# Optimization experiments

Measured on AMD Instinct MI355X. Metric: run time of the kernel, lower is better.

The kernel has to match this reference:

```python
import jax, jax.numpy as jnp
import numpy as np

H = 256
LOG_STD_MIN, LOG_STD_MAX = -20.0, 2.0


def setup_inputs() -> dict:
    key = jax.random.key(0)
    ks = jax.random.split(key, 12)
    B, T, F, A = 256, 1000, 64, 16
    s_in = 1.0 / np.sqrt(H)
    inp = {
        "observations": jax.random.normal(ks[0], (B, T, F), jnp.float32),
        # LSTM params (PyTorch gate order: i, f, g, o)
        "W_ih": jax.random.uniform(ks[1], (4 * H, F), jnp.float32, -s_in, s_in),
        "W_hh": jax.random.uniform(ks[2], (4 * H, H), jnp.float32, -s_in, s_in),
        "b_ih": jax.random.uniform(ks[3], (4 * H,), jnp.float32, -s_in, s_in),
        "b_hh": jax.random.uniform(ks[4], (4 * H,), jnp.float32, -s_in, s_in),
        # layer2: Linear(256 -> 256)
        "W2": jax.random.uniform(ks[5], (H, H), jnp.float32, -s_in, s_in),
        "b2": jax.random.uniform(ks[6], (H,), jnp.float32, -s_in, s_in),
        # means head: Linear(256 -> A)
        "Wm": jax.random.uniform(ks[7], (A, H), jnp.float32, -s_in, s_in),
        "bm": jax.random.uniform(ks[8], (A,), jnp.float32, -s_in, s_in),
        # log_stds head: Linear(256 -> A)
        "Ws": jax.random.uniform(ks[9], (A, H), jnp.float32, -s_in, s_in),
        "bs": jax.random.uniform(ks[10], (A,), jnp.float32, -s_in, s_in),
    }
    return inp


def _lstm(observations, W_ih, W_hh, b_ih, b_hh):
    B, T, F = observations.shape
    # Precompute the input-to-gate projection for all timesteps: [T, B, 4H]
    xg = jnp.einsum("btf,gf->tbg", observations, W_ih) + (b_ih + b_hh)
    W_hh_T = W_hh.T  # [H, 4H]

    def step(carry, xg_t):
        h, c = carry  # [B, H] each
        gates = xg_t + h @ W_hh_T  # [B, 4H]
        i, f, g, o = jnp.split(gates, 4, axis=-1)
        i = jax.nn.sigmoid(i)
        f = jax.nn.sigmoid(f)
        g = jnp.tanh(g)
        o = jax.nn.sigmoid(o)
        c = f * c + i * g
        h = o * jnp.tanh(c)
        return (h, c), h

    h0 = jnp.zeros((B, H), observations.dtype)
    c0 = jnp.zeros((B, H), observations.dtype)
    _, hs = jax.lax.scan(step, (h0, c0), xg)  # hs: [T, B, H]
    return jnp.transpose(hs, (1, 0, 2))  # [B, T, H]


def reference(observations, W_ih, W_hh, b_ih, b_hh, W2, b2, Wm, bm, Ws, bs):
    x = _lstm(observations, W_ih, W_hh, b_ih, b_hh)  # [B, T, H]
    x = jax.nn.relu(jnp.einsum("bth,oh->bto", x, W2) + b2)  # [B, T, H]
    means = jnp.einsum("bth,ah->bta", x, Wm) + bm  # [B, T, A]
    log_stds = jnp.einsum("bth,ah->bta", x, Ws) + bs  # [B, T, A]
    stds = jnp.exp(jnp.clip(log_stds, LOG_STD_MIN, LOG_STD_MAX))
    return (means, stds)
```

## Files before the change

kernel.cpp:

```cpp
#include <hip/hip_runtime.h>


#define NB 256
#define NT 1000
#define NF 64
#define NH 256
#define NG 1024
#define NA 16
#define NTHREADS 512
#define CHUNK 8
#define NCHUNK (NT / CHUNK)
#define HHALF 68

typedef _Float16 h2 __attribute__((ext_vector_type(2)));
typedef _Float16 h4 __attribute__((ext_vector_type(4)));
typedef _Float16 h8 __attribute__((ext_vector_type(8)));
typedef float f4 __attribute__((ext_vector_type(4)));

__device__ __forceinline__ float fdot2(h2 a, h2 b, float c) {
  return __builtin_amdgcn_fdot2(a, b, c, false);
}
__device__ __forceinline__ float fexp2(float x) { return __builtin_amdgcn_exp2f(x); }
__device__ __forceinline__ float frcp(float x) { return __builtin_amdgcn_rcpf(x); }
__device__ __forceinline__ float sigmoidf_(float x) {
  return frcp(1.f + fexp2(-1.4426950408889634f * x));
}
__device__ __forceinline__ float tanhfast(float x) {
  float a = fabsf(x);
  float e = fexp2(-2.8853900817779268f * a);
  float r = (1.f - e) * frcp(1.f + e);
  return __builtin_copysignf(r, x);
}
__device__ __forceinline__ float dot8(h8 x, h8 w, float acc) {
  acc = fdot2(__builtin_shufflevector(x, x, 0, 1), __builtin_shufflevector(w, w, 0, 1), acc);
  acc = fdot2(__builtin_shufflevector(x, x, 2, 3), __builtin_shufflevector(w, w, 2, 3), acc);
  acc = fdot2(__builtin_shufflevector(x, x, 4, 5), __builtin_shufflevector(w, w, 4, 5), acc);
  acc = fdot2(__builtin_shufflevector(x, x, 6, 7), __builtin_shufflevector(w, w, 6, 7), acc);
  return acc;
}
template <int CTRL>
__device__ __forceinline__ float qperm(float x) {
  return __int_as_float(
      __builtin_amdgcn_update_dpp(0, __float_as_int(x), CTRL, 0xF, 0xF, true));
}

__global__ void prep_kernel(const float* __restrict__ Wih, const float* __restrict__ Whh,
                            const float* __restrict__ bih, const float* __restrict__ bhh,
                            const float* __restrict__ W2, const float* __restrict__ Wm,
                            const float* __restrict__ Ws,
                            h2* __restrict__ whh, h2* __restrict__ wih,
                            h2* __restrict__ w2w, h2* __restrict__ wmh,
                            float* __restrict__ bg) {
  int i = blockIdx.x * 256 + threadIdx.x;
  if (i < 1024 * 128) {
    int j = i >> 7, p = i & 127;
    whh[i] = h2{(_Float16)Whh[j * 256 + 2 * p], (_Float16)Whh[j * 256 + 2 * p + 1]};
  }
  if (i < 1024 * 32) {
    int j = i >> 5, p = i & 31;
    wih[i] = h2{(_Float16)Wih[j * 64 + 2 * p], (_Float16)Wih[j * 64 + 2 * p + 1]};
  }
  if (i < 256 * 128) {
    int j = i >> 7, p = i & 127;
    w2w[i] = h2{(_Float16)W2[j * 256 + 2 * p], (_Float16)W2[j * 256 + 2 * p + 1]};
  }
  if (i < 32 * 128) {
    int j = i >> 7, p = i & 127;
    float v0, v1;
    if (j < 16) { v0 = Wm[j * 256 + 2 * p]; v1 = Wm[j * 256 + 2 * p + 1]; }
    else        { v0 = Ws[(j - 16) * 256 + 2 * p]; v1 = Ws[(j - 16) * 256 + 2 * p + 1]; }
    wmh[i] = h2{(_Float16)v0, (_Float16)v1};
  }
  if (i < 1024) bg[i] = bih[i] + bhh[i];
}

__global__ __launch_bounds__(NTHREADS, 2) void actor_kernel(
    const float* __restrict__ obs,
    const h2* __restrict__ whh, const h2* __restrict__ wih,
    const h2* __restrict__ w2w, const h2* __restrict__ wmh,
    const float* __restrict__ bg, const float* __restrict__ b2,
    const float* __restrict__ bm, const float* __restrict__ bs,
    float* __restrict__ out) {
  __shared__ __align__(16) h8 whh_l[16 * NTHREADS];
  __shared__ __align__(16) _Float16 xg_l[CHUNK * NG];
  __shared__ __align__(16) h2 hbuf[2][2 * HHALF];
  __shared__ __align__(16) h2 hch[CHUNK * NH / 2];
  __shared__ __align__(16) h2 xbuf[CHUNK * NF / 2];
  __shared__ __align__(16) h2 x2b[CHUNK * NH / 2];

  const int tid = threadIdx.x;
  const int b = blockIdx.x;
  const int q = tid >> 1;
  const int jhalf = tid & 1;

  h8 wreg[48];
  {
    const volatile h8* vw = (const volatile h8*)whh;
#pragma unroll
    for (int g = 0; g < 4; g++)
#pragma unroll
      for (int jj = 0; jj < 12; jj++)
        wreg[g * 12 + jj] = vw[(g * 256 + q) * 32 + jhalf * 16 + 4 + jj];
  }
  {
    const h8* whh8 = (const h8*)whh;
#pragma unroll
    for (int g = 0; g < 4; g++)
#pragma unroll
      for (int s = 0; s < 4; s++)
        whh_l[(g * 4 + s) * NTHREADS + tid] = whh8[(g * 256 + q) * 32 + jhalf * 16 + s];
  }
  if (tid < 2 * HHALF) hbuf[0][tid] = h2{(_Float16)0.f, (_Float16)0.f};
  float c_state = 0.f;
  const float bg0 = bg[tid], bg1 = bg[tid + 512];
  const float b2v = b2[tid & 255];
  const int oh = tid & 31;
  const float hbv = (oh < NA) ? bm[oh] : bs[oh - NA];
  __syncthreads();

  const float* obs_b = obs + (size_t)b * NT * NF;
  float* out_means = out;
  float* out_stds = out + (size_t)NB * NT * NA;

  for (int ch = 0; ch < NCHUNK; ++ch) {
    const int t0 = ch * CHUNK;

    if (tid < 128) {
      int t = tid >> 4, fq = tid & 15;
      f4 v = *(const f4*)(obs_b + (size_t)(t0 + t) * NF + fq * 4);
      xbuf[t * 32 + fq * 2] = h2{(_Float16)v[0], (_Float16)v[1]};
      xbuf[t * 32 + fq * 2 + 1] = h2{(_Float16)v[2], (_Float16)v[3]};
    }
    __syncthreads();

#pragma unroll
    for (int rr = 0; rr < 2; ++rr) {
      const int row = tid + rr * 512;
      const float bias = rr ? bg1 : bg0;
      float acc[CHUNK];
#pragma unroll
      for (int t = 0; t < CHUNK; t++) acc[t] = bias;
      const h8* wrow = (const h8*)wih + row * 8;
#pragma unroll
      for (int jh = 0; jh < 2; jh++) {
        h8 w[4];
#pragma unroll
        for (int qq = 0; qq < 4; qq++) w[qq] = wrow[jh * 4 + qq];
#pragma unroll
        for (int t = 0; t < CHUNK; t++) {
#pragma unroll
          for (int qq = 0; qq < 4; qq++) {
            h8 xv = *(const h8*)&xbuf[t * 32 + jh * 16 + qq * 4];
            acc[t] = dot8(xv, w[qq], acc[t]);
          }
        }
      }
      const int g = row >> 8, uu = row & 255;
#pragma unroll
      for (int t = 0; t < CHUNK; t++)
        xg_l[(t * 256 + uu) * 4 + g] = (_Float16)acc[t];
    }
    __syncthreads();

    for (int t = 0; t < CHUNK; t++) {
      const _Float16* hb = (const _Float16*)&hbuf[t & 1][jhalf * HHALF];
      h4 xg4 = *(const h4*)&xg_l[(t * 256 + q) * 4];
      float p0 = 0.f, p1 = 0.f, p2 = 0.f, p3 = 0.f;
#pragma unroll
      for (int s = 0; s < 4; s++) {
        h8 hv = *(const h8*)(hb + s * 8);
        p0 = dot8(hv, whh_l[(0 * 4 + s) * NTHREADS + tid], p0);
        p1 = dot8(hv, whh_l[(1 * 4 + s) * NTHREADS + tid], p1);
        p2 = dot8(hv, whh_l[(2 * 4 + s) * NTHREADS + tid], p2);
        p3 = dot8(hv, whh_l[(3 * 4 + s) * NTHREADS + tid], p3);
      }
#pragma unroll
      for (int jj = 0; jj < 12; jj++) {
        h8 hv = *(const h8*)(hb + 32 + jj * 8);
        p0 = dot8(hv, wreg[jj], p0);
        p1 = dot8(hv, wreg[12 + jj], p1);
        p2 = dot8(hv, wreg[24 + jj], p2);
        p3 = dot8(hv, wreg[36 + jj], p3);
      }
      p0 += qperm<0xB1>(p0);
      p1 += qperm<0xB1>(p1);
      p2 += qperm<0xB1>(p2);
      p3 += qperm<0xB1>(p3);
      float gi = sigmoidf_(p0 + (float)xg4[0]);
      float gf = sigmoidf_(p1 + (float)xg4[1]);
      float gg = tanhfast(p2 + (float)xg4[2]);
      float go = sigmoidf_(p3 + (float)xg4[3]);
      c_state = gf * c_state + gi * gg;
      float hval = go * tanhfast(c_state);
      if (jhalf == 0) {
        _Float16 hh = (_Float16)hval;
        ((_Float16*)&hbuf[(t + 1) & 1][(q >> 7) * HHALF])[q & 127] = hh;
        ((_Float16*)hch)[t * NH + q] = hh;
      }
      __syncthreads();
    }

    {
      const int o = tid & 255;
      const int tb = (tid >> 8) * 4;
      float acc[4] = {b2v, b2v, b2v, b2v};
      const h8* wrow = (const h8*)w2w + o * 32;
#pragma unroll 2
      for (int c = 0; c < 8; c++) {
        h8 w[4];
#pragma unroll
        for (int qq = 0; qq < 4; qq++) w[qq] = wrow[c * 4 + qq];
#pragma unroll
        for (int tt = 0; tt < 4; tt++) {
#pragma unroll
          for (int qq = 0; qq < 4; qq++) {
            h8 xv = *(const h8*)&hch[(tb + tt) * 128 + c * 16 + qq * 4];
            acc[tt] = dot8(xv, w[qq], acc[tt]);
          }
        }
      }
#pragma unroll
      for (int tt = 0; tt < 4; tt++)
        ((_Float16*)x2b)[(tb + tt) * NH + o] = (_Float16)fmaxf(acc[tt], 0.f);
    }
    __syncthreads();

    if (tid < 256) {
      const int tt = tid >> 5;
      const h8* wrow = (const h8*)wmh + oh * 32;
      float acc = 0.f;
#pragma unroll 4
      for (int c = 0; c < 32; c++) {
        h8 xv = *(const h8*)&x2b[tt * 128 + c * 4];
        acc = dot8(xv, wrow[c], acc);
      }
      acc += hbv;
      const size_t idx = ((size_t)b * NT + (t0 + tt)) * NA + (oh & 15);
      if (oh < NA) {
        out_means[idx] = acc;
      } else {
        float ls = fminf(fmaxf(acc, -20.f), 2.f);
        out_stds[idx] = fexp2(1.4426950408889634f * ls);
      }
    }
  }
}

extern "C" void kernel_launch(void* const* d_in, const int* in_sizes, int n_in,
                              void* d_out, int out_size, void* d_ws, size_t ws_size,
                              hipStream_t stream) {
  const float* obs = (const float*)d_in[0];
  const float* Wih = (const float*)d_in[1];
  const float* Whh = (const float*)d_in[2];
  const float* bih = (const float*)d_in[3];
  const float* bhh = (const float*)d_in[4];
  const float* W2 = (const float*)d_in[5];
  const float* b2 = (const float*)d_in[6];
  const float* Wm = (const float*)d_in[7];
  const float* bm = (const float*)d_in[8];
  const float* Ws = (const float*)d_in[9];
  const float* bs = (const float*)d_in[10];

  char* ws = (char*)d_ws;
  h2* whh = (h2*)(ws + 0);
  h2* wih = (h2*)(ws + 524288);
  h2* w2w = (h2*)(ws + 655360);
  h2* wmh = (h2*)(ws + 786432);
  float* bg = (float*)(ws + 802816);

  prep_kernel<<<512, 256, 0, stream>>>(Wih, Whh, bih, bhh, W2, Wm, Ws,
                                       whh, wih, w2w, wmh, bg);
  actor_kernel<<<NB, NTHREADS, 0, stream>>>(obs, whh, wih, w2w, wmh, bg, b2, bm,
                                            bs, (float*)d_out);
}
```

Baseline: 4.554 ms.

## Process two batch sequences per block to share recurrent weights and barriers

Each workgroup now runs the LSTM recurrence for two batch rows at once, halving the grid. The recurrent weights held in registers and LDS are reused for both sequences, and each per-timestep barrier covers two sequences, which cuts total synchronisation per sequence. CHUNK drops to 4 so the LDS buffers fit. The cost is twice the dot-product work per step per block and only half the CUs occupied.

```diff
diff --git a/kernel.cpp b/kernel.cpp
--- a/kernel.cpp
+++ b/kernel.cpp
@@ -2,13 +2,14 @@
 
 
 #define NB 256
+#define GRID 128
 #define NT 1000
 #define NF 64
 #define NH 256
 #define NG 1024
 #define NA 16
 #define NTHREADS 512
-#define CHUNK 8
+#define CHUNK 4
 #define NCHUNK (NT / CHUNK)
 #define HHALF 68
 
@@ -82,11 +83,11 @@
     const float* __restrict__ bm, const float* __restrict__ bs,
     float* __restrict__ out) {
   __shared__ __align__(16) h8 whh_l[16 * NTHREADS];
-  __shared__ __align__(16) _Float16 xg_l[CHUNK * NG];
-  __shared__ __align__(16) h2 hbuf[2][2 * HHALF];
-  __shared__ __align__(16) h2 hch[CHUNK * NH / 2];
-  __shared__ __align__(16) h2 xbuf[CHUNK * NF / 2];
-  __shared__ __align__(16) h2 x2b[CHUNK * NH / 2];
+  __shared__ __align__(16) _Float16 xg_l[CHUNK * 2 * NG];
+  __shared__ __align__(16) h2 hbuf[2][2][2 * HHALF];
+  __shared__ __align__(16) h2 hch[2][CHUNK][NH / 2];
+  __shared__ __align__(16) h2 xbuf[2][CHUNK][NF / 2];
+  __shared__ __align__(16) h2 x2b[2][CHUNK][NH / 2];
 
   const int tid = threadIdx.x;
   const int b = blockIdx.x;
@@ -110,15 +111,14 @@
       for (int s = 0; s < 4; s++)
         whh_l[(g * 4 + s) * NTHREADS + tid] = whh8[(g * 256 + q) * 32 + jhalf * 16 + s];
   }
-  if (tid < 2 * HHALF) hbuf[0][tid] = h2{(_Float16)0.f, (_Float16)0.f};
-  float c_state = 0.f;
+  if (tid < 2 * 2 * HHALF) ((h2*)hbuf)[tid] = h2{(_Float16)0.f, (_Float16)0.f};
+  float c0 = 0.f, c1 = 0.f;
   const float bg0 = bg[tid], bg1 = bg[tid + 512];
   const float b2v = b2[tid & 255];
   const int oh = tid & 31;
-  const float hbv = (oh < NA) ? bm[oh] : bs[oh - NA];
+  const float headb = (oh < NA) ? bm[oh] : bs[oh - NA];
   __syncthreads();
 
-  const float* obs_b = obs + (size_t)b * NT * NF;
   float* out_means = out;
   float* out_stds = out + (size_t)NB * NT * NA;
 
@@ -126,10 +126,11 @@
     const int t0 = ch * CHUNK;
 
     if (tid < 128) {
-      int t = tid >> 4, fq = tid & 15;
-      f4 v = *(const f4*)(obs_b + (size_t)(t0 + t) * NF + fq * 4);
-      xbuf[t * 32 + fq * 2] = h2{(_Float16)v[0], (_Float16)v[1]};
-      xbuf[t * 32 + fq * 2 + 1] = h2{(_Float16)v[2], (_Float16)v[3]};
+      int rb = tid >> 6, tq = (tid >> 4) & 3, fq = tid & 15;
+      const float* ob = obs + ((size_t)(2 * b + rb) * NT + (t0 + tq)) * NF;
+      f4 v = *(const f4*)(ob + fq * 4);
+      xbuf[rb][tq][fq * 2] = h2{(_Float16)v[0], (_Float16)v[1]};
+      xbuf[rb][tq][fq * 2 + 1] = h2{(_Float16)v[2], (_Float16)v[3]};
     }
     __syncthreads();
 
@@ -137,9 +138,11 @@
     for (int rr = 0; rr < 2; ++rr) {
       const int row = tid + rr * 512;
       const float bias = rr ? bg1 : bg0;
-      float acc[CHUNK];
-#pragma unroll
-      for (int t = 0; t < CHUNK; t++) acc[t] = bias;
+      float acc[2][4];
+#pragma unroll
+      for (int rb = 0; rb < 2; rb++)
+#pragma unroll
+        for (int tq = 0; tq < 4; tq++) acc[rb][tq] = bias;
       const h8* wrow = (const h8*)wih + row * 8;
 #pragma unroll
       for (int jh = 0; jh < 2; jh++) {
@@ -147,95 +150,123 @@
 #pragma unroll
         for (int qq = 0; qq < 4; qq++) w[qq] = wrow[jh * 4 + qq];
 #pragma unroll
-        for (int t = 0; t < CHUNK; t++) {
-#pragma unroll
-          for (int qq = 0; qq < 4; qq++) {
-            h8 xv = *(const h8*)&xbuf[t * 32 + jh * 16 + qq * 4];
-            acc[t] = dot8(xv, w[qq], acc[t]);
-          }
-        }
+        for (int rb = 0; rb < 2; rb++)
+#pragma unroll
+          for (int tq = 0; tq < 4; tq++)
+#pragma unroll
+            for (int qq = 0; qq < 4; qq++) {
+              h8 xv = *(const h8*)&xbuf[rb][tq][jh * 16 + qq * 4];
+              acc[rb][tq] = dot8(xv, w[qq], acc[rb][tq]);
+            }
       }
       const int g = row >> 8, uu = row & 255;
 #pragma unroll
-      for (int t = 0; t < CHUNK; t++)
-        xg_l[(t * 256 + uu) * 4 + g] = (_Float16)acc[t];
+      for (int rb = 0; rb < 2; rb++)
+#pragma unroll
+        for (int tq = 0; tq < 4; tq++)
+          xg_l[((tq * 2 + rb) * 256 + uu) * 4 + g] = (_Float16)acc[rb][tq];
     }
     __syncthreads();
 
     for (int t = 0; t < CHUNK; t++) {
-      const _Float16* hb = (const _Float16*)&hbuf[t & 1][jhalf * HHALF];
-      h4 xg4 = *(const h4*)&xg_l[(t * 256 + q) * 4];
-      float p0 = 0.f, p1 = 0.f, p2 = 0.f, p3 = 0.f;
+      const _Float16* hbA = (const _Float16*)&hbuf[t & 1][0][jhalf * HHALF];
+      const _Float16* hbB = (const _Float16*)&hbuf[t & 1][1][jhalf * HHALF];
+      h4 xgA = *(const h4*)&xg_l[((t * 2 + 0) * 256 + q) * 4];
+      h4 xgB = *(const h4*)&xg_l[((t * 2 + 1) * 256 + q) * 4];
+      float pa0 = 0.f, pa1 = 0.f, pa2 = 0.f, pa3 = 0.f;
+      float pb0 = 0.f, pb1 = 0.f, pb2 = 0.f, pb3 = 0.f;
 #pragma unroll
       for (int s = 0; s < 4; s++) {
-        h8 hv = *(const h8*)(hb + s * 8);
-        p0 = dot8(hv, whh_l[(0 * 4 + s) * NTHREADS + tid], p0);
-        p1 = dot8(hv, whh_l[(1 * 4 + s) * NTHREADS + tid], p1);
-        p2 = dot8(hv, whh_l[(2 * 4 + s) * NTHREADS + tid], p2);
-        p3 = dot8(hv, whh_l[(3 * 4 + s) * NTHREADS + tid], p3);
+        h8 w0 = whh_l[(0 * 4 + s) * NTHREADS + tid];
+        h8 w1 = whh_l[(1 * 4 + s) * NTHREADS + tid];
+        h8 w2_ = whh_l[(2 * 4 + s) * NTHREADS + tid];
+        h8 w3_ = whh_l[(3 * 4 + s) * NTHREADS + tid];
+        h8 hvA = *(const h8*)(hbA + s * 8);
+        pa0 = dot8(hvA, w0, pa0);
+        pa1 = dot8(hvA, w1, pa1);
+        pa2 = dot8(hvA, w2_, pa2);
+        pa3 = dot8(hvA, w3_, pa3);
+        h8 hvB = *(const h8*)(hbB + s * 8);
+        pb0 = dot8(hvB, w0, pb0);
+        pb1 = dot8(hvB, w1, pb1);
+        pb2 = dot8(hvB, w2_, pb2);
+        pb3 = dot8(hvB, w3_, pb3);
       }
 #pragma unroll
       for (int jj = 0; jj < 12; jj++) {
-        h8 hv = *(const h8*)(hb + 32 + jj * 8);
-        p0 = dot8(hv, wreg[jj], p0);
-        p1 = dot8(hv, wreg[12 + jj], p1);
-        p2 = dot8(hv, wreg[24 + jj], p2);
-        p3 = dot8(hv, wreg[36 + jj], p3);
-      }
-      p0 += qperm<0xB1>(p0);
-      p1 += qperm<0xB1>(p1);
-      p2 += qperm<0xB1>(p2);
-      p3 += qperm<0xB1>(p3);
-      float gi = sigmoidf_(p0 + (float)xg4[0]);
-      float gf = sigmoidf_(p1 + (float)xg4[1]);
-      float gg = tanhfast(p2 + (float)xg4[2]);
-      float go = sigmoidf_(p3 + (float)xg4[3]);
-      c_state = gf * c_state + gi * gg;
-      float hval = go * tanhfast(c_state);
+        h8 hvA = *(const h8*)(hbA + 32 + jj * 8);
+        pa0 = dot8(hvA, wreg[jj], pa0);
+        pa1 = dot8(hvA, wreg[12 + jj], pa1);
+        pa2 = dot8(hvA, wreg[24 + jj], pa2);
+        pa3 = dot8(hvA, wreg[36 + jj], pa3);
+        h8 hvB = *(const h8*)(hbB + 32 + jj * 8);
+        pb0 = dot8(hvB, wreg[jj], pb0);
+        pb1 = dot8(hvB, wreg[12 + jj], pb1);
+        pb2 = dot8(hvB, wreg[24 + jj], pb2);
+        pb3 = dot8(hvB, wreg[36 + jj], pb3);
+      }
+      pa0 += qperm<0xB1>(pa0);
+      pa1 += qperm<0xB1>(pa1);
+      pa2 += qperm<0xB1>(pa2);
+      pa3 += qperm<0xB1>(pa3);
+      pb0 += qperm<0xB1>(pb0);
+      pb1 += qperm<0xB1>(pb1);
+      pb2 += qperm<0xB1>(pb2);
+      pb3 += qperm<0xB1>(pb3);
+      float gi = sigmoidf_(pa0 + (float)xgA[0]);
+      float gf = sigmoidf_(pa1 + (float)xgA[1]);
+      float gg = tanhfast(pa2 + (float)xgA[2]);
+      float go = sigmoidf_(pa3 + (float)xgA[3]);
+      c0 = gf * c0 + gi * gg;
+      float h0 = go * tanhfast(c0);
+      gi = sigmoidf_(pb0 + (float)xgB[0]);
+      gf = sigmoidf_(pb1 + (float)xgB[1]);
+      gg = tanhfast(pb2 + (float)xgB[2]);
+      go = sigmoidf_(pb3 + (float)xgB[3]);
+      c1 = gf * c1 + gi * gg;
+      float h1 = go * tanhfast(c1);
       if (jhalf == 0) {
-        _Float16 hh = (_Float16)hval;
-        ((_Float16*)&hbuf[(t + 1) & 1][(q >> 7) * HHALF])[q & 127] = hh;
-        ((_Float16*)hch)[t * NH + q] = hh;
+        _Float16 ha = (_Float16)h0, hb_ = (_Float16)h1;
+        ((_Float16*)&hbuf[(t + 1) & 1][0][(q >> 7) * HHALF])[q & 127] = ha;
+        ((_Float16*)&hbuf[(t + 1) & 1][1][(q >> 7) * HHALF])[q & 127] = hb_;
+        ((_Float16*)&hch[0][t][0])[q] = ha;
+        ((_Float16*)&hch[1][t][0])[q] = hb_;
       }
       __syncthreads();
     }
 
     {
       const int o = tid & 255;
-      const int tb = (tid >> 8) * 4;
+      const int rb = tid >> 8;
       float acc[4] = {b2v, b2v, b2v, b2v};
       const h8* wrow = (const h8*)w2w + o * 32;
 #pragma unroll 2
-      for (int c = 0; c < 8; c++) {
-        h8 w[4];
-#pragma unroll
-        for (int qq = 0; qq < 4; qq++) w[qq] = wrow[c * 4 + qq];
-#pragma unroll
-        for (int tt = 0; tt < 4; tt++) {
-#pragma unroll
-          for (int qq = 0; qq < 4; qq++) {
-            h8 xv = *(const h8*)&hch[(tb + tt) * 128 + c * 16 + qq * 4];
-            acc[tt] = dot8(xv, w[qq], acc[tt]);
-          }
+      for (int c = 0; c < 32; c++) {
+        h8 w = wrow[c];
+#pragma unroll
+        for (int tq = 0; tq < 4; tq++) {
+          h8 xv = *(const h8*)&hch[rb][tq][c * 4];
+          acc[tq] = dot8(xv, w, acc[tq]);
         }
       }
 #pragma unroll
-      for (int tt = 0; tt < 4; tt++)
-        ((_Float16*)x2b)[(tb + tt) * NH + o] = (_Float16)fmaxf(acc[tt], 0.f);
+      for (int tq = 0; tq < 4; tq++)
+        ((_Float16*)&x2b[rb][tq][0])[o] = (_Float16)fmaxf(acc[tq], 0.f);
     }
     __syncthreads();
 
     if (tid < 256) {
-      const int tt = tid >> 5;
+      const int rb = tid >> 7;
+      const int tt = (tid >> 5) & 3;
       const h8* wrow = (const h8*)wmh + oh * 32;
       float acc = 0.f;
 #pragma unroll 4
       for (int c = 0; c < 32; c++) {
-        h8 xv = *(const h8*)&x2b[tt * 128 + c * 4];
+        h8 xv = *(const h8*)&x2b[rb][tt][c * 4];
         acc = dot8(xv, wrow[c], acc);
       }
-      acc += hbv;
-      const size_t idx = ((size_t)b * NT + (t0 + tt)) * NA + (oh & 15);
+      acc += headb;
+      const size_t idx = ((size_t)(2 * b + rb) * NT + (t0 + tt)) * NA + (oh & 15);
       if (oh < NA) {
         out_means[idx] = acc;
       } else {
@@ -270,6 +301,6 @@
 
   prep_kernel<<<512, 256, 0, stream>>>(Wih, Whh, bih, bhh, W2, Wm, Ws,
                                        whh, wih, w2w, wmh, bg);
-  actor_kernel<<<NB, NTHREADS, 0, stream>>>(obs, whh, wih, w2w, wmh, bg, b2, bm,
-                                            bs, (float*)d_out);
-}
+  actor_kernel<<<GRID, NTHREADS, 0, stream>>>(obs, whh, wih, w2w, wmh, bg, b2,
+                                              bm, bs, (float*)d_out);
+}
```

After: 7.429 ms. +63.1%, slower.

## Interleave input projection for next timestep into recurrent LSTM step loop

Applied to the files above, without the earlier changes.

Removes the per-chunk batched input-to-gate projection phase and its barriers. Each timestep now computes the next timestep's input projection, with W_ih streamed from global through volatile loads, interleaved between the recurrent dot products, and writes it to a double-buffered xg buffer. The observation chunk for the next chunk is prefetched mid-chunk into a double-buffered xbuf. This aims to hide the input GEMM latency inside the latency-bound recurrence, at the cost of re-reading W_ih from global/L2 every timestep instead of reusing it across 8 timesteps, and more register pressure.

```diff
diff --git a/kernel.cpp b/kernel.cpp
--- a/kernel.cpp
+++ b/kernel.cpp
@@ -82,16 +82,17 @@
     const float* __restrict__ bm, const float* __restrict__ bs,
     float* __restrict__ out) {
   __shared__ __align__(16) h8 whh_l[16 * NTHREADS];
-  __shared__ __align__(16) _Float16 xg_l[CHUNK * NG];
+  __shared__ __align__(16) _Float16 xg_db[2][NG];
   __shared__ __align__(16) h2 hbuf[2][2 * HHALF];
   __shared__ __align__(16) h2 hch[CHUNK * NH / 2];
-  __shared__ __align__(16) h2 xbuf[CHUNK * NF / 2];
+  __shared__ __align__(16) h2 xbuf[2][CHUNK][NF / 2];
   __shared__ __align__(16) h2 x2b[CHUNK * NH / 2];
 
   const int tid = threadIdx.x;
   const int b = blockIdx.x;
   const int q = tid >> 1;
   const int jhalf = tid & 1;
+  const int xgi = ((tid & 255) << 2) + (tid >> 8);
 
   h8 wreg[48];
   {
@@ -121,83 +122,120 @@
   const float* obs_b = obs + (size_t)b * NT * NF;
   float* out_means = out;
   float* out_stds = out + (size_t)NB * NT * NA;
+  const volatile h8* vwih = (const volatile h8*)wih;
+
+  if (tid < 128) {
+    int tq = tid >> 4, fq = tid & 15;
+    f4 v = *(const f4*)(obs_b + (size_t)tq * NF + fq * 4);
+    xbuf[0][tq][fq * 2] = h2{(_Float16)v[0], (_Float16)v[1]};
+    xbuf[0][tq][fq * 2 + 1] = h2{(_Float16)v[2], (_Float16)v[3]};
+  }
+  __syncthreads();
+  {
+    float xga = bg0, xgb = bg1;
+#pragma unroll
+    for (int j = 0; j < 8; j++) {
+      h8 wa = vwih[tid * 8 + j];
+      h8 wb = vwih[(tid + 512) * 8 + j];
+      h8 xv = *(const h8*)&xbuf[0][0][j * 4];
+      xga = dot8(xv, wa, xga);
+      xgb = dot8(xv, wb, xgb);
+    }
+    xg_db[0][xgi] = (_Float16)xga;
+    xg_db[0][xgi + 2] = (_Float16)xgb;
+  }
+  __syncthreads();
 
   for (int ch = 0; ch < NCHUNK; ++ch) {
+    const int cb = ch & 1;
     const int t0 = ch * CHUNK;
-
-    if (tid < 128) {
-      int t = tid >> 4, fq = tid & 15;
-      f4 v = *(const f4*)(obs_b + (size_t)(t0 + t) * NF + fq * 4);
-      xbuf[t * 32 + fq * 2] = h2{(_Float16)v[0], (_Float16)v[1]};
-      xbuf[t * 32 + fq * 2 + 1] = h2{(_Float16)v[2], (_Float16)v[3]};
-    }
-    __syncthreads();
-
-#pragma unroll
-    for (int rr = 0; rr < 2; ++rr) {
-      const int row = tid + rr * 512;
-      const float bias = rr ? bg1 : bg0;
-      float acc[CHUNK];
-#pragma unroll
-      for (int t = 0; t < CHUNK; t++) acc[t] = bias;
-      const h8* wrow = (const h8*)wih + row * 8;
-#pragma unroll
-      for (int jh = 0; jh < 2; jh++) {
-        h8 w[4];
-#pragma unroll
-        for (int qq = 0; qq < 4; qq++) w[qq] = wrow[jh * 4 + qq];
-#pragma unroll
-        for (int t = 0; t < CHUNK; t++) {
-#pragma unroll
-          for (int qq = 0; qq < 4; qq++) {
-            h8 xv = *(const h8*)&xbuf[t * 32 + jh * 16 + qq * 4];
-            acc[t] = dot8(xv, w[qq], acc[t]);
-          }
-        }
+    const int chn = (ch + 1 < NCHUNK) ? ch + 1 : ch;
+
+    for (int th = 0; th < CHUNK / 2; th++) {
+#pragma unroll
+      for (int te = 0; te < 2; te++) {
+        const int t = th * 2 + te;
+        const _Float16* hb = (const _Float16*)&hbuf[te][jhalf * HHALF];
+        const _Float16* xsrc = (t < CHUNK - 1)
+                                   ? (const _Float16*)&xbuf[cb][t + 1][0]
+                                   : (const _Float16*)&xbuf[cb ^ 1][0][0];
+        h8 iw0 = vwih[tid * 8 + 0], iw1 = vwih[tid * 8 + 1],
+           iw2 = vwih[tid * 8 + 2], iw3 = vwih[tid * 8 + 3];
+        float p0 = 0.f, p1 = 0.f, p2 = 0.f, p3 = 0.f;
+#pragma unroll
+        for (int s = 0; s < 4; s++) {
+          h8 hv = *(const h8*)(hb + s * 8);
+          p0 = dot8(hv, whh_l[(0 * 4 + s) * NTHREADS + tid], p0);
+          p1 = dot8(hv, whh_l[(1 * 4 + s) * NTHREADS + tid], p1);
+          p2 = dot8(hv, whh_l[(2 * 4 + s) * NTHREADS + tid], p2);
+          p3 = dot8(hv, whh_l[(3 * 4 + s) * NTHREADS + tid], p3);
+        }
+        float xga = bg0;
+        xga = dot8(*(const h8*)(xsrc + 0), iw0, xga);
+        xga = dot8(*(const h8*)(xsrc + 8), iw1, xga);
+        xga = dot8(*(const h8*)(xsrc + 16), iw2, xga);
+        xga = dot8(*(const h8*)(xsrc + 24), iw3, xga);
+        iw0 = vwih[tid * 8 + 4]; iw1 = vwih[tid * 8 + 5];
+        iw2 = vwih[tid * 8 + 6]; iw3 = vwih[tid * 8 + 7];
+#pragma unroll
+        for (int jj = 0; jj < 6; jj++) {
+          h8 hv = *(const h8*)(hb + 32 + jj * 8);
+          p0 = dot8(hv, wreg[jj], p0);
+          p1 = dot8(hv, wreg[12 + jj], p1);
+          p2 = dot8(hv, wreg[24 + jj], p2);
+          p3 = dot8(hv, wreg[36 + jj], p3);
+        }
+        xga = dot8(*(const h8*)(xsrc + 32), iw0, xga);
+        xga = dot8(*(const h8*)(xsrc + 40), iw1, xga);
+        xga = dot8(*(const h8*)(xsrc + 48), iw2, xga);
+        xga = dot8(*(const h8*)(xsrc + 56), iw3, xga);
+        xg_db[te ^ 1][xgi] = (_Float16)xga;
+        iw0 = vwih[(tid + 512) * 8 + 0]; iw1 = vwih[(tid + 512) * 8 + 1];
+        iw2 = vwih[(tid + 512) * 8 + 2]; iw3 = vwih[(tid + 512) * 8 + 3];
+#pragma unroll
+        for (int jj = 6; jj < 12; jj++) {
+          h8 hv = *(const h8*)(hb + 32 + jj * 8);
+          p0 = dot8(hv, wreg[jj], p0);
+          p1 = dot8(hv, wreg[12 + jj], p1);
+          p2 = dot8(hv, wreg[24 + jj], p2);
+          p3 = dot8(hv, wreg[36 + jj], p3);
+        }
+        float xgb = bg1;
+        xgb = dot8(*(const h8*)(xsrc + 0), iw0, xgb);
+        xgb = dot8(*(const h8*)(xsrc + 8), iw1, xgb);
+        xgb = dot8(*(const h8*)(xsrc + 16), iw2, xgb);
+        xgb = dot8(*(const h8*)(xsrc + 24), iw3, xgb);
+        iw0 = vwih[(tid + 512) * 8 + 4]; iw1 = vwih[(tid + 512) * 8 + 5];
+        iw2 = vwih[(tid + 512) * 8 + 6]; iw3 = vwih[(tid + 512) * 8 + 7];
+        p0 += qperm<0xB1>(p0);
+        p1 += qperm<0xB1>(p1);
+        p2 += qperm<0xB1>(p2);
+        p3 += qperm<0xB1>(p3);
+        h4 xg4 = *(const h4*)&xg_db[te][q * 4];
+        float gi = sigmoidf_(p0 + (float)xg4[0]);
+        float gf = sigmoidf_(p1 + (float)xg4[1]);
+        float gg = tanhfast(p2 + (float)xg4[2]);
+        float go = sigmoidf_(p3 + (float)xg4[3]);
+        c_state = gf * c_state + gi * gg;
+        float hval = go * tanhfast(c_state);
+        if (jhalf == 0) {
+          _Float16 hh = (_Float16)hval;
+          ((_Float16*)&hbuf[te ^ 1][(q >> 7) * HHALF])[q & 127] = hh;
+          ((_Float16*)hch)[t * NH + q] = hh;
+        }
+        xgb = dot8(*(const h8*)(xsrc + 32), iw0, xgb);
+        xgb = dot8(*(const h8*)(xsrc + 40), iw1, xgb);
+        xgb = dot8(*(const h8*)(xsrc + 48), iw2, xgb);
+        xgb = dot8(*(const h8*)(xsrc + 56), iw3, xgb);
+        xg_db[te ^ 1][xgi + 2] = (_Float16)xgb;
+        if (te == 0 && th == 2 && tid < 128) {
+          int tq = tid >> 4, fq = tid & 15;
+          f4 v = *(const f4*)(obs_b + ((size_t)chn * CHUNK + tq) * NF + fq * 4);
+          xbuf[cb ^ 1][tq][fq * 2] = h2{(_Float16)v[0], (_Float16)v[1]};
+          xbuf[cb ^ 1][tq][fq * 2 + 1] = h2{(_Float16)v[2], (_Float16)v[3]};
+        }
+        __syncthreads();
       }
-      const int g = row >> 8, uu = row & 255;
-#pragma unroll
-      for (int t = 0; t < CHUNK; t++)
-        xg_l[(t * 256 + uu) * 4 + g] = (_Float16)acc[t];
-    }
-    __syncthreads();
-
-    for (int t = 0; t < CHUNK; t++) {
-      const _Float16* hb = (const _Float16*)&hbuf[t & 1][jhalf * HHALF];
-      h4 xg4 = *(const h4*)&xg_l[(t * 256 + q) * 4];
-      float p0 = 0.f, p1 = 0.f, p2 = 0.f, p3 = 0.f;
-#pragma unroll
-      for (int s = 0; s < 4; s++) {
-        h8 hv = *(const h8*)(hb + s * 8);
-        p0 = dot8(hv, whh_l[(0 * 4 + s) * NTHREADS + tid], p0);
-        p1 = dot8(hv, whh_l[(1 * 4 + s) * NTHREADS + tid], p1);
-        p2 = dot8(hv, whh_l[(2 * 4 + s) * NTHREADS + tid], p2);
-        p3 = dot8(hv, whh_l[(3 * 4 + s) * NTHREADS + tid], p3);
-      }
-#pragma unroll
-      for (int jj = 0; jj < 12; jj++) {
-        h8 hv = *(const h8*)(hb + 32 + jj * 8);
-        p0 = dot8(hv, wreg[jj], p0);
-        p1 = dot8(hv, wreg[12 + jj], p1);
-        p2 = dot8(hv, wreg[24 + jj], p2);
-        p3 = dot8(hv, wreg[36 + jj], p3);
-      }
-      p0 += qperm<0xB1>(p0);
-      p1 += qperm<0xB1>(p1);
-      p2 += qperm<0xB1>(p2);
-      p3 += qperm<0xB1>(p3);
-      float gi = sigmoidf_(p0 + (float)xg4[0]);
-      float gf = sigmoidf_(p1 + (float)xg4[1]);
-      float gg = tanhfast(p2 + (float)xg4[2]);
-      float go = sigmoidf_(p3 + (float)xg4[3]);
-      c_state = gf * c_state + gi * gg;
-      float hval = go * tanhfast(c_state);
-      if (jhalf == 0) {
-        _Float16 hh = (_Float16)hval;
-        ((_Float16*)&hbuf[(t + 1) & 1][(q >> 7) * HHALF])[q & 127] = hh;
-        ((_Float16*)hch)[t * NH + q] = hh;
-      }
-      __syncthreads();
     }
 
     {
```

New measurement: 10.12 ms. 122% more time.
